# Kernel tuning notes

Hardware: AMD Instinct MI355X
Metric: run time of the kernel (lower is better)

Reference implementation:

```python
import jax, jax.numpy as jnp
import numpy as np

N_NODES = 100000


def _add_self_loops(edge_index, n):
    loop = jnp.arange(n, dtype=edge_index.dtype)
    src = jnp.concatenate([edge_index[0], loop])
    dst = jnp.concatenate([edge_index[1], loop])
    return src, dst


def _gcn_conv(x, src, dst, n, W, b):
    # PyG GCNConv: linear first, then sym-normalized aggregation, then bias.
    h = x @ W                                   # [N, out]
    deg = jnp.zeros((n,), h.dtype).at[dst].add(1.0)   # in-degree incl. self-loops
    dinv = jnp.where(deg > 0, jax.lax.rsqrt(deg), 0.0)
    norm = dinv[src] * dinv[dst]                # [E+N]
    msg = h[src] * norm[:, None]                # gather + scale
    out = jax.ops.segment_sum(msg, dst, num_segments=n)  # scatter-add
    return out + b


def setup_inputs() -> dict:
    key = jax.random.key(0)
    ks = jax.random.split(key, 9)
    n, d_in, d_h, d_out = N_NODES, 64, 64, 64
    x = jax.random.normal(ks[0], (n, d_in), jnp.float32)
    edge_index = jax.random.randint(ks[1], (2, 1200000), 0, n, jnp.int64)
    s = lambda k, sh: jax.random.normal(k, sh, jnp.float32) * (1.0 / np.sqrt(sh[0]))
    return {
        "x": x,
        "edge_index": edge_index,
        "W1": s(ks[2], (d_in, d_h)),
        "b1": jnp.zeros((d_h,), jnp.float32),
        "W2": s(ks[3], (d_h, d_out)),
        "b2": jnp.zeros((d_out,), jnp.float32),
        "Wl": s(ks[4], (d_out, d_out)),
        "bl": jnp.zeros((d_out,), jnp.float32),
    }


def reference(x, edge_index, W1, b1, W2, b2, Wl, bl):
    n = x.shape[0]
    src, dst = _add_self_loops(edge_index, n)
    h = _gcn_conv(x, src, dst, n, W1, b1)
    h = jax.nn.relu(h)
    h = _gcn_conv(h, src, dst, n, W2, b2)
    return h @ Wl + bl
```

## Files before the change

### kernel.cpp

```cpp
#include <hip/hip_runtime.h>
#include <hip/hip_bf16.h>


#define FEAT 64
#define CAP 9216

typedef __attribute__((ext_vector_type(8))) short bf16x8;
typedef __attribute__((ext_vector_type(4))) float f32x4;
union BF8 { bf16x8 v; unsigned short u[8]; unsigned pk[4]; uint4 q; };

__device__ __forceinline__ unsigned short f2bf(float f) {
    unsigned u = __float_as_uint(f);
    return (unsigned short)((u + 0x7FFFu + ((u >> 16) & 1u)) >> 16);
}
__device__ __forceinline__ float bflo(unsigned u) { return __uint_as_float(u << 16); }
__device__ __forceinline__ float bfhi(unsigned u) { return __uint_as_float(u & 0xFFFF0000u); }
__device__ __forceinline__ unsigned pk2bf(float a, float b) {
    union { __hip_bfloat162 b; unsigned u; } cv;
    cv.b = __float22bfloat162_rn(make_float2(a, b));
    return cv.u;
}

__global__ void __launch_bounds__(256)
k_part(const int* __restrict__ src, const int* __restrict__ dst,
       int* __restrict__ bcnt, unsigned* __restrict__ buckets, int E, int pblocks,
       const float* __restrict__ W1, const float* __restrict__ W2,
       const float* __restrict__ Wl, unsigned short* __restrict__ P) {
    if ((int)blockIdx.x >= pblocks) {
        int widx = blockIdx.x - pblocks;
        const float* W = (widx == 0) ? W1 : (widx == 1) ? W2 : Wl;
        unsigned short* p = P + widx * 4096;
        for (int i = threadIdx.x; i < 4096; i += 256) {
            int c = i >> 10, s = (i >> 9) & 1, l = (i >> 3) & 63, j = i & 7;
            int k = s * 32 + ((l >> 4) << 3) + j;
            int col = ((l & 15) << 2) + c;
            p[i] = f2bf(W[k * 64 + col]);
        }
        return;
    }
    __shared__ unsigned pk[4096];
    __shared__ unsigned char bk[4096];
    __shared__ int h[256];
    __shared__ int cur[256];
    int tid = threadIdx.x;
    h[tid] = 0;
    __syncthreads();
    int base = blockIdx.x * 4096;
#pragma unroll
    for (int i = 0; i < 16; ++i) {
        int li = i * 256 + tid;
        int e = base + li;
        if (e < E) {
            int s = src[e], d = dst[e];
            int b = d >> 9;
            pk[li] = ((unsigned)s << 9) | ((unsigned)d & 511u);
            bk[li] = (unsigned char)b;
            atomicAdd(&h[b], 1);
        } else {
            bk[li] = 255;
        }
    }
    __syncthreads();
    {
        int c = h[tid];
        int run = c ? atomicAdd(&bcnt[tid], c) : 0;
        cur[tid] = run;
    }
    __syncthreads();
#pragma unroll
    for (int i = 0; i < 16; ++i) {
        int li = i * 256 + tid;
        int e = base + li;
        if (e < E) {
            int b = bk[li];
            int pos = atomicAdd(&cur[b], 1);
            buckets[(size_t)b * CAP + pos] = pk[li];
        }
    }
}

__global__ void __launch_bounds__(512)
k_csr(const unsigned* __restrict__ buckets, const int* __restrict__ bcnt,
      const float* __restrict__ x, const unsigned short* __restrict__ Wpk,
      unsigned short* __restrict__ Hs1, int* __restrict__ esrc,
      int* __restrict__ perm, int2* __restrict__ pofs, float* __restrict__ pdinv,
      int n) {
    __shared__ int hist[512];
    __shared__ int cur[512];
    __shared__ int dh[64];
    __shared__ int dbase[64];
    __shared__ int dcur[64];
    __shared__ float sdinv[512];
    int tid = threadIdx.x;
    int b = blockIdx.x;
    hist[tid] = 0;
    if (tid < 64) dh[tid] = 0;
    __syncthreads();
    int cnt = bcnt[b];
    size_t beg = (size_t)b * CAP;
    for (int j = tid; j < cnt; j += 512)
        atomicAdd(&hist[buckets[beg + j] & 511u], 1);
    __syncthreads();
    int v = hist[tid];
    for (int off = 1; off < 512; off <<= 1) {
        int xs = (tid >= off) ? hist[tid - off] : 0;
        __syncthreads();
        hist[tid] += xs;
        __syncthreads();
    }
    int excl = hist[tid] - v;
    int node = (b << 9) + tid;
    bool valid = node < n;
    float di = rsqrtf((float)v + 1.0f);
    sdinv[tid] = di;
    if (valid) atomicAdd(&dh[min(v, 63)], 1);
    cur[tid] = excl;
    __syncthreads();
    if (tid == 0) {
        int run = 0;
        for (int i = 0; i < 64; ++i) { dbase[i] = run; run += dh[i]; dcur[i] = 0; }
    }
    __syncthreads();
    if (valid) {
        int bin = min(v, 63);
        int r = atomicAdd(&dcur[bin], 1);
        int gs = (b << 9) + dbase[bin] + r;
        perm[gs] = node;
        pofs[gs] = make_int2((int)beg + excl, (int)beg + excl + v);
        pdinv[gs] = di;
    }
    for (int j = tid; j < cnt; j += 512) {
        unsigned u = buckets[beg + j];
        int loc = (int)(u & 511u);
        int r = atomicAdd(&cur[loc], 1);
        esrc[beg + r] = (int)(u >> 9);
    }
    int lane = tid & 63;
    int wv = tid >> 6;
    BF8 bfr[8];
    const uint4* wp = (const uint4*)Wpk;
#pragma unroll
    for (int f = 0; f < 8; ++f) bfr[f].q = wp[f * 64 + lane];
    int mrow = lane & 15, kq = lane >> 4, colb = lane & 15;
    for (int t = wv; t < 32; t += 8) {
        int rb = (b << 9) + (t << 4);
        int row = rb + mrow;
        bool ok = row < n;
        BF8 a0, a1;
        const float4* xr = (const float4*)(x + ((unsigned)row << 6));
        float4 z = make_float4(0.f, 0.f, 0.f, 0.f);
        float4 p0 = ok ? xr[kq * 2]     : z;
        float4 p1 = ok ? xr[kq * 2 + 1] : z;
        float4 p2 = ok ? xr[8 + kq * 2] : z;
        float4 p3 = ok ? xr[8 + kq * 2 + 1] : z;
        a0.pk[0] = pk2bf(p0.x, p0.y); a0.pk[1] = pk2bf(p0.z, p0.w);
        a0.pk[2] = pk2bf(p1.x, p1.y); a0.pk[3] = pk2bf(p1.z, p1.w);
        a1.pk[0] = pk2bf(p2.x, p2.y); a1.pk[1] = pk2bf(p2.z, p2.w);
        a1.pk[2] = pk2bf(p3.x, p3.y); a1.pk[3] = pk2bf(p3.z, p3.w);
        f32x4 acc0 = {0.f, 0.f, 0.f, 0.f}, acc1 = acc0, acc2 = acc0, acc3 = acc0;
        acc0 = __builtin_amdgcn_mfma_f32_16x16x32_bf16(a0.v, bfr[0].v, acc0, 0, 0, 0);
        acc0 = __builtin_amdgcn_mfma_f32_16x16x32_bf16(a1.v, bfr[1].v, acc0, 0, 0, 0);
        acc1 = __builtin_amdgcn_mfma_f32_16x16x32_bf16(a0.v, bfr[2].v, acc1, 0, 0, 0);
        acc1 = __builtin_amdgcn_mfma_f32_16x16x32_bf16(a1.v, bfr[3].v, acc1, 0, 0, 0);
        acc2 = __builtin_amdgcn_mfma_f32_16x16x32_bf16(a0.v, bfr[4].v, acc2, 0, 0, 0);
        acc2 = __builtin_amdgcn_mfma_f32_16x16x32_bf16(a1.v, bfr[5].v, acc2, 0, 0, 0);
        acc3 = __builtin_amdgcn_mfma_f32_16x16x32_bf16(a0.v, bfr[6].v, acc3, 0, 0, 0);
        acc3 = __builtin_amdgcn_mfma_f32_16x16x32_bf16(a1.v, bfr[7].v, acc3, 0, 0, 0);
        int rowb = rb + (kq << 2);
        int lrow = (t << 4) + (kq << 2);
#pragma unroll
        for (int i = 0; i < 4; ++i) {
            if (rowb + i >= n) break;
            float sc = sdinv[lrow + i];
            unsigned ro = (unsigned)(rowb + i) << 6;
            uint2 o = make_uint2(pk2bf(acc0[i] * sc, acc1[i] * sc),
                                 pk2bf(acc2[i] * sc, acc3[i] * sc));
            *(uint2*)(Hs1 + ro + (colb << 2)) = o;
        }
    }
}

__device__ __forceinline__ int slot_of(int q, int B, int r) {
    return (q << 9) + ((r >> 3) << 7) + (B << 3) + (r & 7);
}

#define ACC8(H, W) \
    a0 = fmaf(bflo(H.x), W, a0); a1 = fmaf(bfhi(H.x), W, a1); \
    a2 = fmaf(bflo(H.y), W, a2); a3 = fmaf(bfhi(H.y), W, a3); \
    a4 = fmaf(bflo(H.z), W, a4); a5 = fmaf(bfhi(H.z), W, a5); \
    a6 = fmaf(bflo(H.w), W, a6); a7 = fmaf(bfhi(H.w), W, a7);

#define GROW(s) (*(const uint4*)(Hs + ((unsigned)(s) << 6) + (h8 << 3)))

#define HALF(hX0, hX1, hX2, hX3, sX0, sX1, sX2, sX3, wX0, wX1, wX2, wX3)  \
    {                                                                     \
        int jn = j + 8;                                                   \
        int n0 = sX0, n1 = sX1, n2 = sX2, n3 = sX3;                       \
        float v0 = 0.f, v1 = 0.f, v2 = 0.f, v3 = 0.f;                     \
        if (jn     < end) { n0 = esrc[jn];     v0 = 1.f; }                \
        if (jn + 1 < end) { n1 = esrc[jn + 1]; v1 = 1.f; }                \
        if (jn + 2 < end) { n2 = esrc[jn + 2]; v2 = 1.f; }                \
        if (jn + 3 < end) { n3 = esrc[jn + 3]; v3 = 1.f; }                \
        ACC8(hX0, wX0) ACC8(hX1, wX1) ACC8(hX2, wX2) ACC8(hX3, wX3)       \
        hX0 = GROW(n0); hX1 = GROW(n1); hX2 = GROW(n2); hX3 = GROW(n3);   \
        sX0 = n0; sX1 = n1; sX2 = n2; sX3 = n3;                           \
        wX0 = v0; wX1 = v1; wX2 = v2; wX3 = v3;                           \
        j += 4;                                                           \
    }

template <bool RELU, bool OUT_F32>
__global__ void __launch_bounds__(256)
k_fagg(const int* __restrict__ perm, const int2* __restrict__ pofs,
       const float* __restrict__ pdinv, const int* __restrict__ esrc,
       const unsigned short* __restrict__ Hs, const float* __restrict__ bias1,
       const unsigned short* __restrict__ Wpk, const float* __restrict__ bias2,
       void* __restrict__ outv, int n) {
    __shared__ uint4 lds_a[32][8];
    int tid = threadIdx.x;
    int lane = tid & 63;
    int wv = tid >> 6;
    int h8 = lane & 7;
    int q = blockIdx.x >> 4, B = blockIdx.x & 15;
    int rl = (wv << 3) + (lane >> 3);
    int slot = slot_of(q, B, rl);
    bool ok = slot < n;
    int node = 0, beg = 0, end = 0;
    float dd = 0.f;
    if (ok) {
        node = perm[slot];
        int2 oe = pofs[slot];
        beg = oe.x; end = oe.y;
        dd = pdinv[slot];
    }
    float a0 = 0.f, a1 = 0.f, a2 = 0.f, a3 = 0.f, a4 = 0.f, a5 = 0.f, a6 = 0.f, a7 = 0.f;
    {
        int j = beg;
        int sA0 = 0, sA1 = 0, sA2 = 0, sA3 = 0;
        float wA0 = 0.f, wA1 = 0.f, wA2 = 0.f, wA3 = 0.f;
        if (j     < end) { sA0 = esrc[j];     wA0 = 1.f; }
        if (j + 1 < end) { sA1 = esrc[j + 1]; wA1 = 1.f; }
        if (j + 2 < end) { sA2 = esrc[j + 2]; wA2 = 1.f; }
        if (j + 3 < end) { sA3 = esrc[j + 3]; wA3 = 1.f; }
        int sB0 = sA0, sB1 = sA1, sB2 = sA2, sB3 = sA3;
        float wB0 = 0.f, wB1 = 0.f, wB2 = 0.f, wB3 = 0.f;
        if (j + 4 < end) { sB0 = esrc[j + 4]; wB0 = 1.f; }
        if (j + 5 < end) { sB1 = esrc[j + 5]; wB1 = 1.f; }
        if (j + 6 < end) { sB2 = esrc[j + 6]; wB2 = 1.f; }
        if (j + 7 < end) { sB3 = esrc[j + 7]; wB3 = 1.f; }
        uint4 hA0 = GROW(sA0), hA1 = GROW(sA1), hA2 = GROW(sA2), hA3 = GROW(sA3);
        uint4 hB0 = GROW(sB0), hB1 = GROW(sB1), hB2 = GROW(sB2), hB3 = GROW(sB3);
        while (__ballot(j < end)) {
            HALF(hA0, hA1, hA2, hA3, sA0, sA1, sA2, sA3, wA0, wA1, wA2, wA3)
            if (!__ballot(j < end)) break;
            HALF(hB0, hB1, hB2, hB3, sB0, sB1, sB2, sB3, wB0, wB1, wB2, wB3)
        }
    }
    uint4 packed = make_uint4(0, 0, 0, 0);
    if (ok) {
        uint4 sv = *(const uint4*)(Hs + ((unsigned)node << 6) + (h8 << 3));
        const float4* b4 = (const float4*)bias1;
        float4 bA = b4[h8 * 2], bB = b4[h8 * 2 + 1];
        float r0 = (a0 + bflo(sv.x)) * dd + bA.x;
        float r1 = (a1 + bfhi(sv.x)) * dd + bA.y;
        float r2 = (a2 + bflo(sv.y)) * dd + bA.z;
        float r3 = (a3 + bfhi(sv.y)) * dd + bA.w;
        float r4 = (a4 + bflo(sv.z)) * dd + bB.x;
        float r5 = (a5 + bfhi(sv.z)) * dd + bB.y;
        float r6 = (a6 + bflo(sv.w)) * dd + bB.z;
        float r7 = (a7 + bfhi(sv.w)) * dd + bB.w;
        if (RELU) {
            r0 = fmaxf(r0, 0.f); r1 = fmaxf(r1, 0.f); r2 = fmaxf(r2, 0.f); r3 = fmaxf(r3, 0.f);
            r4 = fmaxf(r4, 0.f); r5 = fmaxf(r5, 0.f); r6 = fmaxf(r6, 0.f); r7 = fmaxf(r7, 0.f);
        }
        packed = make_uint4(pk2bf(r0, r1), pk2bf(r2, r3), pk2bf(r4, r5), pk2bf(r6, r7));
    }
    lds_a[rl][h8 ^ (rl & 7)] = packed;
    __syncthreads();
    int hh = wv & 1, tt = wv >> 1;
    BF8 bq0, bq1, bq2, bq3;
    {
        const uint4* wp = (const uint4*)Wpk;
        bq0.q = wp[(4 * hh + 0) * 64 + lane];
        bq1.q = wp[(4 * hh + 1) * 64 + lane];
        bq2.q = wp[(4 * hh + 2) * 64 + lane];
        bq3.q = wp[(4 * hh + 3) * 64 + lane];
    }
    int mr = lane & 15, kq = lane >> 4, colb = lane & 15;
    int rloc = tt * 16 + mr;
    BF8 fa0, fa1;
    fa0.q = lds_a[rloc][kq ^ (rloc & 7)];
    fa1.q = lds_a[rloc][(kq + 4) ^ (rloc & 7)];
    f32x4 accA = {0.f, 0.f, 0.f, 0.f}, accB = accA;
    accA = __builtin_amdgcn_mfma_f32_16x16x32_bf16(fa0.v, bq0.v, accA, 0, 0, 0);
    accA = __builtin_amdgcn_mfma_f32_16x16x32_bf16(fa1.v, bq1.v, accA, 0, 0, 0);
    accB = __builtin_amdgcn_mfma_f32_16x16x32_bf16(fa0.v, bq2.v, accB, 0, 0, 0);
    accB = __builtin_amdgcn_mfma_f32_16x16x32_bf16(fa1.v, bq3.v, accB, 0, 0, 0);
    float b2x = 0.f, b2y = 0.f;
    if (OUT_F32) {
        b2x = bias2[(colb << 2) + (hh << 1)];
        b2y = bias2[(colb << 2) + (hh << 1) + 1];
    }
    int rowb = tt * 16 + (kq << 2);
#pragma unroll
    for (int i = 0; i < 4; ++i) {
        int sl = slot_of(q, B, rowb + i);
        if (sl >= n) continue;
        int orow = perm[sl];
        if (OUT_F32) {
            float2 o = make_float2(accA[i] + b2x, accB[i] + b2y);
            *(float2*)((float*)outv + ((unsigned)orow << 6) + (colb << 2) + (hh << 1)) = o;
        } else {
            float sc = pdinv[sl];
            unsigned o = pk2bf(accA[i] * sc, accB[i] * sc);
            *(unsigned*)((unsigned short*)outv + ((unsigned)orow << 6) + (colb << 2) + (hh << 1)) = o;
        }
    }
}

extern "C" void kernel_launch(void* const* d_in, const int* in_sizes, int n_in,
                              void* d_out, int out_size, void* d_ws, size_t ws_size,
                              hipStream_t stream) {
    const float* x  = (const float*)d_in[0];
    const int*   ei = (const int*)d_in[1];
    const float* W1 = (const float*)d_in[2];
    const float* b1 = (const float*)d_in[3];
    const float* W2 = (const float*)d_in[4];
    const float* b2 = (const float*)d_in[5];
    const float* Wl = (const float*)d_in[6];
    const float* bl = (const float*)d_in[7];
    float* out = (float*)d_out;

    const int n = in_sizes[0] / FEAT;
    const int E = in_sizes[1] / 2;
    const int* src = ei;
    const int* dst = ei + E;

    const int B = 256;
    const int NB = (n + 511) >> 9;
    const int pblocks = (E + 4095) / 4096;
    const int fagg_blocks = NB * 16;

    char* w = (char*)d_ws;
    int*   bcnt     = (int*)w;              w += 256 * 4;
    float* pdinv    = (float*)w;            w += (size_t)n * 4;
    int*   perm     = (int*)w;              w += (size_t)n * 4;
    w = (char*)(((uintptr_t)w + 15) & ~(uintptr_t)15);
    int2*  pofs     = (int2*)w;             w += (size_t)n * 8;
    unsigned short* Wpk = (unsigned short*)w;  w += 3 * 4096 * 2;
    w = (char*)(((uintptr_t)w + 15) & ~(uintptr_t)15);
    unsigned* buckets = (unsigned*)w;       w += (size_t)NB * CAP * 4;
    int*   esrc     = (int*)w;              w += (size_t)NB * CAP * 4;
    unsigned short* bufA = (unsigned short*)w;  w += (size_t)n * FEAT * 2;
    unsigned short* bufB = (unsigned short*)w;

    hipMemsetAsync(bcnt, 0, 256 * 4, stream);
    k_part<<<dim3(pblocks + 3), dim3(B), 0, stream>>>(src, dst, bcnt, buckets, E,
                                                      pblocks, W1, W2, Wl, Wpk);
    k_csr<<<dim3(NB), dim3(512), 0, stream>>>(buckets, bcnt, x, Wpk, bufA,
                                              esrc, perm, pofs, pdinv, n);

    k_fagg<true, false><<<dim3(fagg_blocks), dim3(B), 0, stream>>>(
        perm, pofs, pdinv, esrc, bufA, b1, Wpk + 4096, nullptr, bufB, n);

    k_fagg<false, true><<<dim3(fagg_blocks), dim3(B), 0, stream>>>(
        perm, pofs, pdinv, esrc, bufB, b2, Wpk + 8192, bl, out, n);
}
```

Before: 205.2 us.

## Decouple first GEMM from CSR blocks and use atomic work queues

Per-node in-degree is now counted in the partition kernel with global atomics. This lets the x@W1 GEMM in k_csr compute its normalization without the block-local histogram. k_csr launches 1024 blocks: only the first NB build the CSR, and all blocks pull 16-row GEMM tiles from a global atomic counter. Both aggregation kernels become persistent 2048-block loops that fetch work units from atomic counters. The aim is better load balance and CU utilization, at the cost of 1.2M extra global atomics and per-unit counter and sync overhead.

```diff
diff --git a/kernel.cpp b/kernel.cpp
--- a/kernel.cpp
+++ b/kernel.cpp
@@ -23,7 +23,8 @@
 
 __global__ void __launch_bounds__(256)
 k_part(const int* __restrict__ src, const int* __restrict__ dst,
-       int* __restrict__ bcnt, unsigned* __restrict__ buckets, int E, int pblocks,
+       int* __restrict__ bcnt, int* __restrict__ ndeg,
+       unsigned* __restrict__ buckets, int E, int pblocks,
        const float* __restrict__ W1, const float* __restrict__ W2,
        const float* __restrict__ Wl, unsigned short* __restrict__ P) {
     if ((int)blockIdx.x >= pblocks) {
@@ -56,6 +57,7 @@
             pk[li] = ((unsigned)s << 9) | ((unsigned)d & 511u);
             bk[li] = (unsigned char)b;
             atomicAdd(&h[b], 1);
+            atomicAdd(&ndeg[d], 1);
         } else {
             bk[li] = 255;
         }
@@ -81,69 +83,72 @@
 
 __global__ void __launch_bounds__(512)
 k_csr(const unsigned* __restrict__ buckets, const int* __restrict__ bcnt,
+      const int* __restrict__ ndeg, int* __restrict__ gctr,
       const float* __restrict__ x, const unsigned short* __restrict__ Wpk,
       unsigned short* __restrict__ Hs1, int* __restrict__ esrc,
       int* __restrict__ perm, int2* __restrict__ pofs, float* __restrict__ pdinv,
-      int n) {
+      int n, int nb, int ntiles) {
     __shared__ int hist[512];
     __shared__ int cur[512];
     __shared__ int dh[64];
     __shared__ int dbase[64];
     __shared__ int dcur[64];
-    __shared__ float sdinv[512];
     int tid = threadIdx.x;
     int b = blockIdx.x;
-    hist[tid] = 0;
-    if (tid < 64) dh[tid] = 0;
-    __syncthreads();
-    int cnt = bcnt[b];
-    size_t beg = (size_t)b * CAP;
-    for (int j = tid; j < cnt; j += 512)
-        atomicAdd(&hist[buckets[beg + j] & 511u], 1);
-    __syncthreads();
-    int v = hist[tid];
-    for (int off = 1; off < 512; off <<= 1) {
-        int xs = (tid >= off) ? hist[tid - off] : 0;
-        __syncthreads();
-        hist[tid] += xs;
-        __syncthreads();
-    }
-    int excl = hist[tid] - v;
-    int node = (b << 9) + tid;
-    bool valid = node < n;
-    float di = rsqrtf((float)v + 1.0f);
-    sdinv[tid] = di;
-    if (valid) atomicAdd(&dh[min(v, 63)], 1);
-    cur[tid] = excl;
-    __syncthreads();
-    if (tid == 0) {
-        int run = 0;
-        for (int i = 0; i < 64; ++i) { dbase[i] = run; run += dh[i]; dcur[i] = 0; }
-    }
-    __syncthreads();
-    if (valid) {
-        int bin = min(v, 63);
-        int r = atomicAdd(&dcur[bin], 1);
-        int gs = (b << 9) + dbase[bin] + r;
-        perm[gs] = node;
-        pofs[gs] = make_int2((int)beg + excl, (int)beg + excl + v);
-        pdinv[gs] = di;
-    }
-    for (int j = tid; j < cnt; j += 512) {
-        unsigned u = buckets[beg + j];
-        int loc = (int)(u & 511u);
-        int r = atomicAdd(&cur[loc], 1);
-        esrc[beg + r] = (int)(u >> 9);
+    if (b < nb) {
+        hist[tid] = 0;
+        if (tid < 64) dh[tid] = 0;
+        __syncthreads();
+        int cnt = bcnt[b];
+        size_t beg = (size_t)b * CAP;
+        for (int j = tid; j < cnt; j += 512)
+            atomicAdd(&hist[buckets[beg + j] & 511u], 1);
+        __syncthreads();
+        int v = hist[tid];
+        for (int off = 1; off < 512; off <<= 1) {
+            int xs = (tid >= off) ? hist[tid - off] : 0;
+            __syncthreads();
+            hist[tid] += xs;
+            __syncthreads();
+        }
+        int excl = hist[tid] - v;
+        int node = (b << 9) + tid;
+        bool valid = node < n;
+        if (valid) atomicAdd(&dh[min(v, 63)], 1);
+        cur[tid] = excl;
+        __syncthreads();
+        if (tid == 0) {
+            int run = 0;
+            for (int i = 0; i < 64; ++i) { dbase[i] = run; run += dh[i]; dcur[i] = 0; }
+        }
+        __syncthreads();
+        if (valid) {
+            int bin = min(v, 63);
+            int r = atomicAdd(&dcur[bin], 1);
+            int gs = (b << 9) + dbase[bin] + r;
+            perm[gs] = node;
+            pofs[gs] = make_int2((int)beg + excl, (int)beg + excl + v);
+            pdinv[gs] = rsqrtf((float)v + 1.0f);
+        }
+        for (int j = tid; j < cnt; j += 512) {
+            unsigned u = buckets[beg + j];
+            int loc = (int)(u & 511u);
+            int r = atomicAdd(&cur[loc], 1);
+            esrc[beg + r] = (int)(u >> 9);
+        }
     }
     int lane = tid & 63;
-    int wv = tid >> 6;
     BF8 bfr[8];
     const uint4* wp = (const uint4*)Wpk;
 #pragma unroll
     for (int f = 0; f < 8; ++f) bfr[f].q = wp[f * 64 + lane];
     int mrow = lane & 15, kq = lane >> 4, colb = lane & 15;
-    for (int t = wv; t < 32; t += 8) {
-        int rb = (b << 9) + (t << 4);
+    for (;;) {
+        int t;
+        if (lane == 0) t = atomicAdd(gctr, 1);
+        t = __shfl(t, 0);
+        if (t >= ntiles) break;
+        int rb = t << 4;
         int row = rb + mrow;
         bool ok = row < n;
         BF8 a0, a1;
@@ -167,11 +172,10 @@
         acc3 = __builtin_amdgcn_mfma_f32_16x16x32_bf16(a0.v, bfr[6].v, acc3, 0, 0, 0);
         acc3 = __builtin_amdgcn_mfma_f32_16x16x32_bf16(a1.v, bfr[7].v, acc3, 0, 0, 0);
         int rowb = rb + (kq << 2);
-        int lrow = (t << 4) + (kq << 2);
 #pragma unroll
         for (int i = 0; i < 4; ++i) {
             if (rowb + i >= n) break;
-            float sc = sdinv[lrow + i];
+            float sc = rsqrtf((float)ndeg[rowb + i] + 1.0f);
             unsigned ro = (unsigned)(rowb + i) << 6;
             uint2 o = make_uint2(pk2bf(acc0[i] * sc, acc1[i] * sc),
                                  pk2bf(acc2[i] * sc, acc3[i] * sc));
@@ -214,105 +218,112 @@
        const float* __restrict__ pdinv, const int* __restrict__ esrc,
        const unsigned short* __restrict__ Hs, const float* __restrict__ bias1,
        const unsigned short* __restrict__ Wpk, const float* __restrict__ bias2,
-       void* __restrict__ outv, int n) {
+       void* __restrict__ outv, int* __restrict__ ctr, int nunits, int n) {
     __shared__ uint4 lds_a[32][8];
+    __shared__ int s_unit;
     int tid = threadIdx.x;
     int lane = tid & 63;
     int wv = tid >> 6;
     int h8 = lane & 7;
-    int q = blockIdx.x >> 4, B = blockIdx.x & 15;
     int rl = (wv << 3) + (lane >> 3);
-    int slot = slot_of(q, B, rl);
-    bool ok = slot < n;
-    int node = 0, beg = 0, end = 0;
-    float dd = 0.f;
-    if (ok) {
-        node = perm[slot];
-        int2 oe = pofs[slot];
-        beg = oe.x; end = oe.y;
-        dd = pdinv[slot];
-    }
-    float a0 = 0.f, a1 = 0.f, a2 = 0.f, a3 = 0.f, a4 = 0.f, a5 = 0.f, a6 = 0.f, a7 = 0.f;
-    {
-        int j = beg;
-        int sA0 = 0, sA1 = 0, sA2 = 0, sA3 = 0;
-        float wA0 = 0.f, wA1 = 0.f, wA2 = 0.f, wA3 = 0.f;
-        if (j     < end) { sA0 = esrc[j];     wA0 = 1.f; }
-        if (j + 1 < end) { sA1 = esrc[j + 1]; wA1 = 1.f; }
-        if (j + 2 < end) { sA2 = esrc[j + 2]; wA2 = 1.f; }
-        if (j + 3 < end) { sA3 = esrc[j + 3]; wA3 = 1.f; }
-        int sB0 = sA0, sB1 = sA1, sB2 = sA2, sB3 = sA3;
-        float wB0 = 0.f, wB1 = 0.f, wB2 = 0.f, wB3 = 0.f;
-        if (j + 4 < end) { sB0 = esrc[j + 4]; wB0 = 1.f; }
-        if (j + 5 < end) { sB1 = esrc[j + 5]; wB1 = 1.f; }
-        if (j + 6 < end) { sB2 = esrc[j + 6]; wB2 = 1.f; }
-        if (j + 7 < end) { sB3 = esrc[j + 7]; wB3 = 1.f; }
-        uint4 hA0 = GROW(sA0), hA1 = GROW(sA1), hA2 = GROW(sA2), hA3 = GROW(sA3);
-        uint4 hB0 = GROW(sB0), hB1 = GROW(sB1), hB2 = GROW(sB2), hB3 = GROW(sB3);
-        while (__ballot(j < end)) {
-            HALF(hA0, hA1, hA2, hA3, sA0, sA1, sA2, sA3, wA0, wA1, wA2, wA3)
-            if (!__ballot(j < end)) break;
-            HALF(hB0, hB1, hB2, hB3, sB0, sB1, sB2, sB3, wB0, wB1, wB2, wB3)
-        }
-    }
-    uint4 packed = make_uint4(0, 0, 0, 0);
-    if (ok) {
-        uint4 sv = *(const uint4*)(Hs + ((unsigned)node << 6) + (h8 << 3));
-        const float4* b4 = (const float4*)bias1;
-        float4 bA = b4[h8 * 2], bB = b4[h8 * 2 + 1];
-        float r0 = (a0 + bflo(sv.x)) * dd + bA.x;
-        float r1 = (a1 + bfhi(sv.x)) * dd + bA.y;
-        float r2 = (a2 + bflo(sv.y)) * dd + bA.z;
-        float r3 = (a3 + bfhi(sv.y)) * dd + bA.w;
-        float r4 = (a4 + bflo(sv.z)) * dd + bB.x;
-        float r5 = (a5 + bfhi(sv.z)) * dd + bB.y;
-        float r6 = (a6 + bflo(sv.w)) * dd + bB.z;
-        float r7 = (a7 + bfhi(sv.w)) * dd + bB.w;
-        if (RELU) {
-            r0 = fmaxf(r0, 0.f); r1 = fmaxf(r1, 0.f); r2 = fmaxf(r2, 0.f); r3 = fmaxf(r3, 0.f);
-            r4 = fmaxf(r4, 0.f); r5 = fmaxf(r5, 0.f); r6 = fmaxf(r6, 0.f); r7 = fmaxf(r7, 0.f);
-        }
-        packed = make_uint4(pk2bf(r0, r1), pk2bf(r2, r3), pk2bf(r4, r5), pk2bf(r6, r7));
-    }
-    lds_a[rl][h8 ^ (rl & 7)] = packed;
-    __syncthreads();
-    int hh = wv & 1, tt = wv >> 1;
-    BF8 bq0, bq1, bq2, bq3;
-    {
-        const uint4* wp = (const uint4*)Wpk;
-        bq0.q = wp[(4 * hh + 0) * 64 + lane];
-        bq1.q = wp[(4 * hh + 1) * 64 + lane];
-        bq2.q = wp[(4 * hh + 2) * 64 + lane];
-        bq3.q = wp[(4 * hh + 3) * 64 + lane];
-    }
-    int mr = lane & 15, kq = lane >> 4, colb = lane & 15;
-    int rloc = tt * 16 + mr;
-    BF8 fa0, fa1;
-    fa0.q = lds_a[rloc][kq ^ (rloc & 7)];
-    fa1.q = lds_a[rloc][(kq + 4) ^ (rloc & 7)];
-    f32x4 accA = {0.f, 0.f, 0.f, 0.f}, accB = accA;
-    accA = __builtin_amdgcn_mfma_f32_16x16x32_bf16(fa0.v, bq0.v, accA, 0, 0, 0);
-    accA = __builtin_amdgcn_mfma_f32_16x16x32_bf16(fa1.v, bq1.v, accA, 0, 0, 0);
-    accB = __builtin_amdgcn_mfma_f32_16x16x32_bf16(fa0.v, bq2.v, accB, 0, 0, 0);
-    accB = __builtin_amdgcn_mfma_f32_16x16x32_bf16(fa1.v, bq3.v, accB, 0, 0, 0);
-    float b2x = 0.f, b2y = 0.f;
-    if (OUT_F32) {
-        b2x = bias2[(colb << 2) + (hh << 1)];
-        b2y = bias2[(colb << 2) + (hh << 1) + 1];
-    }
-    int rowb = tt * 16 + (kq << 2);
-#pragma unroll
-    for (int i = 0; i < 4; ++i) {
-        int sl = slot_of(q, B, rowb + i);
-        if (sl >= n) continue;
-        int orow = perm[sl];
+    for (;;) {
+        if (tid == 0) s_unit = atomicAdd(ctr, 1);
+        __syncthreads();
+        int unit = s_unit;
+        if (unit >= nunits) break;
+        int q = unit >> 4, B = unit & 15;
+        int slot = slot_of(q, B, rl);
+        bool ok = slot < n;
+        int node = 0, beg = 0, end = 0;
+        float dd = 0.f;
+        if (ok) {
+            node = perm[slot];
+            int2 oe = pofs[slot];
+            beg = oe.x; end = oe.y;
+            dd = pdinv[slot];
+        }
+        float a0 = 0.f, a1 = 0.f, a2 = 0.f, a3 = 0.f, a4 = 0.f, a5 = 0.f, a6 = 0.f, a7 = 0.f;
+        {
+            int j = beg;
+            int sA0 = 0, sA1 = 0, sA2 = 0, sA3 = 0;
+            float wA0 = 0.f, wA1 = 0.f, wA2 = 0.f, wA3 = 0.f;
+            if (j     < end) { sA0 = esrc[j];     wA0 = 1.f; }
+            if (j + 1 < end) { sA1 = esrc[j + 1]; wA1 = 1.f; }
+            if (j + 2 < end) { sA2 = esrc[j + 2]; wA2 = 1.f; }
+            if (j + 3 < end) { sA3 = esrc[j + 3]; wA3 = 1.f; }
+            int sB0 = sA0, sB1 = sA1, sB2 = sA2, sB3 = sA3;
+            float wB0 = 0.f, wB1 = 0.f, wB2 = 0.f, wB3 = 0.f;
+            if (j + 4 < end) { sB0 = esrc[j + 4]; wB0 = 1.f; }
+            if (j + 5 < end) { sB1 = esrc[j + 5]; wB1 = 1.f; }
+            if (j + 6 < end) { sB2 = esrc[j + 6]; wB2 = 1.f; }
+            if (j + 7 < end) { sB3 = esrc[j + 7]; wB3 = 1.f; }
+            uint4 hA0 = GROW(sA0), hA1 = GROW(sA1), hA2 = GROW(sA2), hA3 = GROW(sA3);
+            uint4 hB0 = GROW(sB0), hB1 = GROW(sB1), hB2 = GROW(sB2), hB3 = GROW(sB3);
+            while (__ballot(j < end)) {
+                HALF(hA0, hA1, hA2, hA3, sA0, sA1, sA2, sA3, wA0, wA1, wA2, wA3)
+                if (!__ballot(j < end)) break;
+                HALF(hB0, hB1, hB2, hB3, sB0, sB1, sB2, sB3, wB0, wB1, wB2, wB3)
+            }
+        }
+        uint4 packed = make_uint4(0, 0, 0, 0);
+        if (ok) {
+            uint4 sv = *(const uint4*)(Hs + ((unsigned)node << 6) + (h8 << 3));
+            const float4* b4 = (const float4*)bias1;
+            float4 bA = b4[h8 * 2], bB = b4[h8 * 2 + 1];
+            float r0 = (a0 + bflo(sv.x)) * dd + bA.x;
+            float r1 = (a1 + bfhi(sv.x)) * dd + bA.y;
+            float r2 = (a2 + bflo(sv.y)) * dd + bA.z;
+            float r3 = (a3 + bfhi(sv.y)) * dd + bA.w;
+            float r4 = (a4 + bflo(sv.z)) * dd + bB.x;
+            float r5 = (a5 + bfhi(sv.z)) * dd + bB.y;
+            float r6 = (a6 + bflo(sv.w)) * dd + bB.z;
+            float r7 = (a7 + bfhi(sv.w)) * dd + bB.w;
+            if (RELU) {
+                r0 = fmaxf(r0, 0.f); r1 = fmaxf(r1, 0.f); r2 = fmaxf(r2, 0.f); r3 = fmaxf(r3, 0.f);
+                r4 = fmaxf(r4, 0.f); r5 = fmaxf(r5, 0.f); r6 = fmaxf(r6, 0.f); r7 = fmaxf(r7, 0.f);
+            }
+            packed = make_uint4(pk2bf(r0, r1), pk2bf(r2, r3), pk2bf(r4, r5), pk2bf(r6, r7));
+        }
+        lds_a[rl][h8 ^ (rl & 7)] = packed;
+        __syncthreads();
+        int hh = wv & 1, tt = wv >> 1;
+        BF8 bq0, bq1, bq2, bq3;
+        {
+            const uint4* wp = (const uint4*)Wpk;
+            bq0.q = wp[(4 * hh + 0) * 64 + lane];
+            bq1.q = wp[(4 * hh + 1) * 64 + lane];
+            bq2.q = wp[(4 * hh + 2) * 64 + lane];
+            bq3.q = wp[(4 * hh + 3) * 64 + lane];
+        }
+        int mr = lane & 15, kq = lane >> 4, colb = lane & 15;
+        int rloc = tt * 16 + mr;
+        BF8 fa0, fa1;
+        fa0.q = lds_a[rloc][kq ^ (rloc & 7)];
+        fa1.q = lds_a[rloc][(kq + 4) ^ (rloc & 7)];
+        f32x4 accA = {0.f, 0.f, 0.f, 0.f}, accB = accA;
+        accA = __builtin_amdgcn_mfma_f32_16x16x32_bf16(fa0.v, bq0.v, accA, 0, 0, 0);
+        accA = __builtin_amdgcn_mfma_f32_16x16x32_bf16(fa1.v, bq1.v, accA, 0, 0, 0);
+        accB = __builtin_amdgcn_mfma_f32_16x16x32_bf16(fa0.v, bq2.v, accB, 0, 0, 0);
+        accB = __builtin_amdgcn_mfma_f32_16x16x32_bf16(fa1.v, bq3.v, accB, 0, 0, 0);
+        float b2x = 0.f, b2y = 0.f;
         if (OUT_F32) {
-            float2 o = make_float2(accA[i] + b2x, accB[i] + b2y);
-            *(float2*)((float*)outv + ((unsigned)orow << 6) + (colb << 2) + (hh << 1)) = o;
-        } else {
-            float sc = pdinv[sl];
-            unsigned o = pk2bf(accA[i] * sc, accB[i] * sc);
-            *(unsigned*)((unsigned short*)outv + ((unsigned)orow << 6) + (colb << 2) + (hh << 1)) = o;
+            b2x = bias2[(colb << 2) + (hh << 1)];
+            b2y = bias2[(colb << 2) + (hh << 1) + 1];
+        }
+        int rowb = tt * 16 + (kq << 2);
+#pragma unroll
+        for (int i = 0; i < 4; ++i) {
+            int sl = slot_of(q, B, rowb + i);
+            if (sl >= n) continue;
+            int orow = perm[sl];
+            if (OUT_F32) {
+                float2 o = make_float2(accA[i] + b2x, accB[i] + b2y);
+                *(float2*)((float*)outv + ((unsigned)orow << 6) + (colb << 2) + (hh << 1)) = o;
+            } else {
+                float sc = pdinv[sl];
+                unsigned o = pk2bf(accA[i] * sc, accB[i] * sc);
+                *(unsigned*)((unsigned short*)outv + ((unsigned)orow << 6) + (colb << 2) + (hh << 1)) = o;
+            }
         }
     }
 }
@@ -338,10 +349,15 @@
     const int B = 256;
     const int NB = (n + 511) >> 9;
     const int pblocks = (E + 4095) / 4096;
-    const int fagg_blocks = NB * 16;
+    const int nunits = NB * 16;
+    const int ntiles = (n + 15) >> 4;
 
     char* w = (char*)d_ws;
-    int*   bcnt     = (int*)w;              w += 256 * 4;
+    int*   bcnt     = (int*)w;
+    int*   ctrs     = bcnt + 256;
+    int*   ndeg     = bcnt + 260;
+    size_t zwords   = 260 + (size_t)n;
+    w += zwords * 4;
     float* pdinv    = (float*)w;            w += (size_t)n * 4;
     int*   perm     = (int*)w;              w += (size_t)n * 4;
     w = (char*)(((uintptr_t)w + 15) & ~(uintptr_t)15);
@@ -353,15 +369,21 @@
     unsigned short* bufA = (unsigned short*)w;  w += (size_t)n * FEAT * 2;
     unsigned short* bufB = (unsigned short*)w;
 
-    hipMemsetAsync(bcnt, 0, 256 * 4, stream);
-    k_part<<<dim3(pblocks + 3), dim3(B), 0, stream>>>(src, dst, bcnt, buckets, E,
-                                                      pblocks, W1, W2, Wl, Wpk);
-    k_csr<<<dim3(NB), dim3(512), 0, stream>>>(buckets, bcnt, x, Wpk, bufA,
-                                              esrc, perm, pofs, pdinv, n);
-
-    k_fagg<true, false><<<dim3(fagg_blocks), dim3(B), 0, stream>>>(
-        perm, pofs, pdinv, esrc, bufA, b1, Wpk + 4096, nullptr, bufB, n);
-
-    k_fagg<false, true><<<dim3(fagg_blocks), dim3(B), 0, stream>>>(
-        perm, pofs, pdinv, esrc, bufB, b2, Wpk + 8192, bl, out, n);
-}
+    hipMemsetAsync(bcnt, 0, zwords * 4, stream);
+
+    k_part<<<dim3(pblocks + 3), dim3(B), 0, stream>>>(src, dst, bcnt, ndeg,
+                                                      buckets, E, pblocks,
+                                                      W1, W2, Wl, Wpk);
+
+    k_csr<<<dim3(1024), dim3(512), 0, stream>>>(buckets, bcnt, ndeg, &ctrs[0],
+                                                x, Wpk, bufA, esrc,
+                                                perm, pofs, pdinv, n, NB, ntiles);
+
+    k_fagg<true, false><<<dim3(2048), dim3(B), 0, stream>>>(
+        perm, pofs, pdinv, esrc, bufA, b1, Wpk + 4096, nullptr, bufB,
+        &ctrs[1], nunits, n);
+
+    k_fagg<false, true><<<dim3(2048), dim3(B), 0, stream>>>(
+        perm, pofs, pdinv, esrc, bufB, b2, Wpk + 8192, bl, out,
+        &ctrs[2], nunits, n);
+}
```

Result: slower. 481.6 us (+134.7%).
